# Performance work log

Hardware: AMD Instinct MI355X
Metric: run time of the kernel (lower is better)

## Reference

```python
import jax, jax.numpy as jnp
import numpy as np

INPUT_SIZE = 75
HIDDEN = 128
NUM_CLASSES = 10

def setup_inputs() -> dict:
    key = jax.random.key(0)
    ks = jax.random.split(key, 8)
    B, T = 512, 512
    s_ih = 1.0 / np.sqrt(HIDDEN)
    x = jax.random.normal(ks[0], (B, T, INPUT_SIZE), dtype=jnp.float32)
    w_ih = jax.random.uniform(ks[1], (4 * HIDDEN, INPUT_SIZE), jnp.float32, -s_ih, s_ih)
    w_hh = jax.random.uniform(ks[2], (4 * HIDDEN, HIDDEN), jnp.float32, -s_ih, s_ih)
    b_ih = jax.random.uniform(ks[3], (4 * HIDDEN,), jnp.float32, -s_ih, s_ih)
    b_hh = jax.random.uniform(ks[4], (4 * HIDDEN,), jnp.float32, -s_ih, s_ih)
    fc_w = jax.random.uniform(ks[5], (NUM_CLASSES, HIDDEN), jnp.float32, -s_ih, s_ih)
    fc_b = jax.random.uniform(ks[6], (NUM_CLASSES,), jnp.float32, -s_ih, s_ih)
    return {"x": x, "w_ih": w_ih, "w_hh": w_hh, "b_ih": b_ih, "b_hh": b_hh, "fc_w": fc_w, "fc_b": fc_b}

def _lstm_last_h(x, w_ih, w_hh, b_ih, b_hh):
    # x: [B, T, I]. Precompute input contribution once: [B, T, 4H]
    xg = jnp.einsum('bti,gi->btg', x, w_ih) + b_ih + b_hh
    B = x.shape[0]
    h0 = jnp.zeros((B, HIDDEN), x.dtype)
    c0 = jnp.zeros((B, HIDDEN), x.dtype)

    def step(carry, xg_t):
        h, c = carry
        gates = xg_t + h @ w_hh.T  # [B, 4H]
        i, f, g, o = jnp.split(gates, 4, axis=-1)  # torch gate order i,f,g,o
        i = jax.nn.sigmoid(i)
        f = jax.nn.sigmoid(f)
        g = jnp.tanh(g)
        o = jax.nn.sigmoid(o)
        c = f * c + i * g
        h = o * jnp.tanh(c)
        return (h, c), None

    (h, c), _ = jax.lax.scan(step, (h0, c0), jnp.swapaxes(xg, 0, 1))
    return h  # last hidden state [B, H]

def reference(x, w_ih, w_hh, b_ih, b_hh, fc_w, fc_b):
    h_n = _lstm_last_h(x, w_ih, w_hh, b_ih, b_hh)
    return h_n @ fc_w.T + fc_b  # [B, 10]
```

## Files before the change

### kernel.cpp

```cpp
#include <hip/hip_runtime.h>
#include <hip/hip_bf16.h>

#define HID 128
#define ISZ 75
#define KDIM 224
#define KC 7
#define TT 512
#define BB 512
#define ZSTR 232

typedef _Float16 half8 __attribute__((ext_vector_type(8)));
typedef float floatx4 __attribute__((ext_vector_type(4)));

__device__ __forceinline__ float rcp_fast(float x) { return __builtin_amdgcn_rcpf(x); }
__device__ __forceinline__ float sigmoid_f(float x) { return rcp_fast(1.f + __expf(-x)); }
__device__ __forceinline__ float tanh_f(float x) { return 1.f - 2.f * rcp_fast(__expf(2.f * x) + 1.f); }

__global__ __launch_bounds__(1024, 1) void lstm_mfma(
    const float* __restrict__ x,
    const float* __restrict__ w_ih,
    const float* __restrict__ w_hh,
    const float* __restrict__ b_ih,
    const float* __restrict__ b_hh,
    const float* __restrict__ fc_w,
    const float* __restrict__ fc_b,
    float* __restrict__ out)
{
    const int tid  = threadIdx.x;
    const int wave = tid >> 6;
    const int lane = tid & 63;
    const int l15  = lane & 15;
    const int l4   = lane >> 4;
    const int b0   = blockIdx.x * 2;
    const int wb   = wave * 32;

    __shared__ __align__(16) _Float16 zsh[16][ZSTR];
    __shared__ __align__(16) float    psh[2][512];

    {
        int* zi = (int*)&zsh[0][0];
        const int n4 = 16 * ZSTR / 2;
        for (int i = tid; i < n4; i += 1024) zi[i] = 0;
    }
    __syncthreads();

    if (tid >= 256 && tid < 256 + 2 * ISZ) {
        int u = tid - 256;
        int nb = (u >= ISZ) ? 1 : 0;
        int k = u - nb * ISZ;
        zsh[nb][HID + k] = (_Float16)x[((size_t)(b0 + nb) * TT) * ISZ + k];
    }

    half8  wfr[2][KC];
    floatx4 bias[2];
#pragma unroll
    for (int mt = 0; mt < 2; ++mt) {
        const int R = wb + mt * 16 + l15;
#pragma unroll
        for (int kc = 0; kc < KC; ++kc) {
            half8 f;
            const int kbase = kc * 32 + l4 * 8;
#pragma unroll
            for (int e = 0; e < 8; ++e) {
                const int k = kbase + e;
                float v = 0.f;
                if (k < HID)            v = w_hh[R * HID + k];
                else if (k < HID + ISZ) v = w_ih[R * ISZ + (k - HID)];
                f[e] = (_Float16)v;
            }
            wfr[mt][kc] = f;
        }
        floatx4 bf;
#pragma unroll
        for (int j = 0; j < 4; ++j) {
            const int g = wb + mt * 16 + l4 * 4 + j;
            bf[j] = b_ih[g] + b_hh[g];
        }
        bias[mt] = bf;
    }

    float c = 0.f;
    __syncthreads();

#pragma unroll 1
    for (int t = 0; t < TT; ++t) {
        float xpre = 0.f;
        int xnb = 0, xk = 0;
        const bool xthr = (tid >= 256 && tid < 256 + 2 * ISZ);
        if (xthr) {
            int u = tid - 256;
            xnb = (u >= ISZ) ? 1 : 0;
            xk = u - xnb * ISZ;
            int tn = (t + 1 < TT) ? (t + 1) : t;
            xpre = x[((size_t)(b0 + xnb) * TT + tn) * ISZ + xk];
        }

        floatx4 acc0 = bias[0], acc1 = bias[1];
#pragma unroll
        for (int kc = 0; kc < KC; ++kc) {
            half8 z = *(const half8*)&zsh[l15][kc * 32 + l4 * 8];
            acc0 = __builtin_amdgcn_mfma_f32_16x16x32_f16(wfr[0][kc], z, acc0, 0, 0, 0);
            acc1 = __builtin_amdgcn_mfma_f32_16x16x32_f16(wfr[1][kc], z, acc1, 0, 0, 0);
        }
        if (l15 < 2) {
            *(floatx4*)&psh[l15][wb + l4 * 4]      = acc0;
            *(floatx4*)&psh[l15][wb + 16 + l4 * 4] = acc1;
        }
        __syncthreads();

        if (tid < 256) {
            const int nb = tid >> 7, j = tid & 127;
            float pi = psh[nb][j];
            float pf = psh[nb][HID + j];
            float pg = psh[nb][2 * HID + j];
            float po = psh[nb][3 * HID + j];
            float ig = sigmoid_f(pi);
            float fg = sigmoid_f(pf);
            float gg = tanh_f(pg);
            float og = sigmoid_f(po);
            c = fmaf(fg, c, ig * gg);
            zsh[nb][j] = (_Float16)(og * tanh_f(c));
        } else if (xthr && (t + 1 < TT)) {
            zsh[xnb][HID + xk] = (_Float16)xpre;
        }
        __syncthreads();
    }

    if (tid < 20) {
        const int nb = tid / 10, k = tid - nb * 10;
        float s = fc_b[k];
        const float* w = fc_w + k * HID;
#pragma unroll
        for (int d = 0; d < HID; ++d) s = fmaf(w[d], (float)zsh[nb][d], s);
        out[(b0 + nb) * 10 + k] = s;
    }
}

extern "C" void kernel_launch(void* const* d_in, const int* in_sizes, int n_in,
                              void* d_out, int out_size, void* d_ws, size_t ws_size,
                              hipStream_t stream) {
    const float* x    = (const float*)d_in[0];
    const float* w_ih = (const float*)d_in[1];
    const float* w_hh = (const float*)d_in[2];
    const float* b_ih = (const float*)d_in[3];
    const float* b_hh = (const float*)d_in[4];
    const float* fc_w = (const float*)d_in[5];
    const float* fc_b = (const float*)d_in[6];
    float* out = (float*)d_out;

    lstm_mfma<<<dim3(BB / 2), dim3(1024), 0, stream>>>(
        x, w_ih, w_hh, b_ih, b_hh, fc_w, fc_b, out);
}
```

Before: 601.0 us.

## Precompute input projection with a separate GEMM kernel and shrink recurrent K

Adds an xg_gemm kernel that computes x·W_ih^T plus both biases for all timesteps into an fp16 workspace buffer. The recurrent kernel then only runs MFMAs over the 128-wide hidden state (4 K-chunks instead of 7) and prefetches the precomputed gate inputs two steps ahead. Hidden state in LDS moves to a chunk-interleaved layout. The cost is a 256 MB fp16 intermediate write and read through HBM, plus an extra kernel launch. The old fused kernel stays as a fallback when the workspace is too small.

```diff
diff --git a/kernel.cpp b/kernel.cpp
--- a/kernel.cpp
+++ b/kernel.cpp
@@ -3,36 +3,208 @@
 
 #define HID 128
 #define ISZ 75
-#define KDIM 224
-#define KC 7
+#define GATES 512
 #define TT 512
 #define BB 512
-#define ZSTR 232
 
 typedef _Float16 half8 __attribute__((ext_vector_type(8)));
+typedef _Float16 half4 __attribute__((ext_vector_type(4)));
 typedef float floatx4 __attribute__((ext_vector_type(4)));
 
 __device__ __forceinline__ float rcp_fast(float x) { return __builtin_amdgcn_rcpf(x); }
 __device__ __forceinline__ float sigmoid_f(float x) { return rcp_fast(1.f + __expf(-x)); }
 __device__ __forceinline__ float tanh_f(float x) { return 1.f - 2.f * rcp_fast(__expf(2.f * x) + 1.f); }
 
-__global__ __launch_bounds__(1024, 1) void lstm_mfma(
+__global__ __launch_bounds__(256, 2) void xg_gemm(
     const float* __restrict__ x,
     const float* __restrict__ w_ih,
-    const float* __restrict__ w_hh,
     const float* __restrict__ b_ih,
     const float* __restrict__ b_hh,
+    _Float16* __restrict__ xg)
+{
+    const int tid = threadIdx.x;
+    const int wv = tid >> 6, lane = tid & 63;
+    const int l15 = lane & 15, l4 = lane >> 4;
+
+    __shared__ __align__(16) _Float16 wlds[12 * 256 * 8];
+    __shared__ __align__(16) float    xlds[64 * ISZ];
+
+    const size_t rowblk = (size_t)blockIdx.x * 512;
+
+    for (int nh = 0; nh < 2; ++nh) {
+        const int gbase = nh * 256;
+        {
+            const float* wrow = w_ih + (size_t)(gbase + tid) * ISZ;
+            for (int k = 0; k < 96; ++k) {
+                float v = (k < ISZ) ? wrow[k] : 0.f;
+                wlds[((k >> 3) * 256 + tid) * 8 + (k & 7)] = (_Float16)v;
+            }
+        }
+        float biasv[16];
+#pragma unroll
+        for (int nt = 0; nt < 16; ++nt) {
+            int g = gbase + nt * 16 + l15;
+            biasv[nt] = b_ih[g] + b_hh[g];
+        }
+        __syncthreads();
+
+        for (int mt = 0; mt < 8; ++mt) {
+            const size_t r0 = rowblk + (size_t)mt * 64;
+            {
+                const float4* src = (const float4*)(x + r0 * ISZ);
+                float4* dst = (float4*)xlds;
+                for (int i = tid; i < 1200; i += 256) dst[i] = src[i];
+            }
+            __syncthreads();
+
+            half8 af[3];
+#pragma unroll
+            for (int kc = 0; kc < 3; ++kc) {
+                const int rb = (wv * 16 + l15) * ISZ;
+                half8 f;
+#pragma unroll
+                for (int e = 0; e < 8; ++e) {
+                    int k = kc * 32 + l4 * 8 + e;
+                    int kk = (k < ISZ) ? k : 0;
+                    float v = xlds[rb + kk];
+                    f[e] = (_Float16)((k < ISZ) ? v : 0.f);
+                }
+                af[kc] = f;
+            }
+
+            floatx4 acc[16];
+#pragma unroll
+            for (int nt = 0; nt < 16; ++nt)
+                acc[nt] = (floatx4){biasv[nt], biasv[nt], biasv[nt], biasv[nt]};
+#pragma unroll
+            for (int kc = 0; kc < 3; ++kc) {
+                const int cb = (kc * 4 + l4) * 256;
+#pragma unroll
+                for (int nt = 0; nt < 16; ++nt) {
+                    half8 bf = *(const half8*)&wlds[(cb + nt * 16 + l15) * 8];
+                    acc[nt] = __builtin_amdgcn_mfma_f32_16x16x32_f16(af[kc], bf, acc[nt], 0, 0, 0);
+                }
+            }
+
+            _Float16* orow = xg + (r0 + wv * 16 + l4 * 4) * GATES + gbase + l15;
+#pragma unroll
+            for (int nt = 0; nt < 16; ++nt) {
+#pragma unroll
+                for (int j = 0; j < 4; ++j)
+                    orow[(size_t)j * GATES + nt * 16] = (_Float16)acc[nt][j];
+            }
+            __syncthreads();
+        }
+        __syncthreads();
+    }
+}
+
+__global__ __launch_bounds__(1024, 1) void lstm_rec(
+    const _Float16* __restrict__ xg,
+    const float* __restrict__ w_hh,
     const float* __restrict__ fc_w,
     const float* __restrict__ fc_b,
     float* __restrict__ out)
 {
-    const int tid  = threadIdx.x;
-    const int wave = tid >> 6;
-    const int lane = tid & 63;
-    const int l15  = lane & 15;
-    const int l4   = lane >> 4;
-    const int b0   = blockIdx.x * 2;
-    const int wb   = wave * 32;
+    const int tid = threadIdx.x;
+    const int wave = tid >> 6, lane = tid & 63;
+    const int l15 = lane & 15, l4 = lane >> 4;
+    const int b0 = blockIdx.x * 2;
+    const int wb = wave * 32;
+
+    __shared__ __align__(16) _Float16 zsh[16 * 16 * 8];
+    __shared__ __align__(16) float    psh[2][GATES];
+
+    half8 wfr[2][4];
+#pragma unroll
+    for (int mt = 0; mt < 2; ++mt) {
+        const int R = wb + mt * 16 + l15;
+#pragma unroll
+        for (int kc = 0; kc < 4; ++kc) {
+            half8 f;
+#pragma unroll
+            for (int e = 0; e < 8; ++e)
+                f[e] = (_Float16)w_hh[R * HID + kc * 32 + l4 * 8 + e];
+            wfr[mt][kc] = f;
+        }
+    }
+    for (int i = tid; i < 16 * 16 * 8 / 2; i += 1024) ((uint32_t*)zsh)[i] = 0;
+
+    float c = 0.f;
+    const bool ldact = (l15 < 2);
+    const _Float16* xgp = xg + ((size_t)(b0 + (l15 & 1)) * TT) * GATES + wb + l4 * 4;
+
+    half4 xgA0, xgA1, xgB0, xgB1;
+    if (ldact) {
+        xgA0 = *(const half4*)(xgp);
+        xgA1 = *(const half4*)(xgp + 16);
+        xgB0 = *(const half4*)(xgp + GATES);
+        xgB1 = *(const half4*)(xgp + GATES + 16);
+    }
+    __syncthreads();
+
+    auto step = [&](half4& xq0, half4& xq1, int tpre) {
+        floatx4 acc0, acc1;
+#pragma unroll
+        for (int j = 0; j < 4; ++j) { acc0[j] = (float)xq0[j]; acc1[j] = (float)xq1[j]; }
+        if (ldact) {
+            const _Float16* p = xgp + (size_t)tpre * GATES;
+            xq0 = *(const half4*)(p);
+            xq1 = *(const half4*)(p + 16);
+        }
+#pragma unroll
+        for (int kc = 0; kc < 4; ++kc) {
+            half8 z = *(const half8*)&zsh[((kc * 4 + l4) * 16 + l15) * 8];
+            acc0 = __builtin_amdgcn_mfma_f32_16x16x32_f16(wfr[0][kc], z, acc0, 0, 0, 0);
+            acc1 = __builtin_amdgcn_mfma_f32_16x16x32_f16(wfr[1][kc], z, acc1, 0, 0, 0);
+        }
+        if (ldact) {
+            *(floatx4*)&psh[l15][wb + l4 * 4]      = acc0;
+            *(floatx4*)&psh[l15][wb + 16 + l4 * 4] = acc1;
+        }
+        __syncthreads();
+        if (tid < 256) {
+            const int nb = tid >> 7, j = tid & 127;
+            float ig = sigmoid_f(psh[nb][j]);
+            float fg = sigmoid_f(psh[nb][HID + j]);
+            float gg = tanh_f(psh[nb][2 * HID + j]);
+            float og = sigmoid_f(psh[nb][3 * HID + j]);
+            c = fmaf(fg, c, ig * gg);
+            zsh[((j >> 3) * 16 + nb) * 8 + (j & 7)] = (_Float16)(og * tanh_f(c));
+        }
+        __syncthreads();
+    };
+
+#pragma unroll 1
+    for (int t = 0; t < TT; t += 2) {
+        step(xgA0, xgA1, (t + 2 < TT) ? t + 2 : TT - 1);
+        step(xgB0, xgB1, (t + 3 < TT) ? t + 3 : TT - 1);
+    }
+
+    if (tid < 20) {
+        const int nb = tid / 10, k = tid - nb * 10;
+        float s = fc_b[k];
+        const float* w = fc_w + k * HID;
+#pragma unroll
+        for (int d = 0; d < HID; ++d)
+            s = fmaf(w[d], (float)zsh[((d >> 3) * 16 + nb) * 8 + (d & 7)], s);
+        out[(b0 + nb) * 10 + k] = s;
+    }
+}
+
+#define KC7 7
+#define ZSTR 232
+__global__ __launch_bounds__(1024, 1) void lstm_mfma(
+    const float* __restrict__ x, const float* __restrict__ w_ih,
+    const float* __restrict__ w_hh, const float* __restrict__ b_ih,
+    const float* __restrict__ b_hh, const float* __restrict__ fc_w,
+    const float* __restrict__ fc_b, float* __restrict__ out)
+{
+    const int tid = threadIdx.x;
+    const int wave = tid >> 6, lane = tid & 63;
+    const int l15 = lane & 15, l4 = lane >> 4;
+    const int b0 = blockIdx.x * 2;
+    const int wb = wave * 32;
 
     __shared__ __align__(16) _Float16 zsh[16][ZSTR];
     __shared__ __align__(16) float    psh[2][512];
@@ -43,21 +215,19 @@
         for (int i = tid; i < n4; i += 1024) zi[i] = 0;
     }
     __syncthreads();
-
     if (tid >= 256 && tid < 256 + 2 * ISZ) {
         int u = tid - 256;
         int nb = (u >= ISZ) ? 1 : 0;
         int k = u - nb * ISZ;
         zsh[nb][HID + k] = (_Float16)x[((size_t)(b0 + nb) * TT) * ISZ + k];
     }
-
-    half8  wfr[2][KC];
+    half8 wfr[2][KC7];
     floatx4 bias[2];
 #pragma unroll
     for (int mt = 0; mt < 2; ++mt) {
         const int R = wb + mt * 16 + l15;
 #pragma unroll
-        for (int kc = 0; kc < KC; ++kc) {
+        for (int kc = 0; kc < KC7; ++kc) {
             half8 f;
             const int kbase = kc * 32 + l4 * 8;
 #pragma unroll
@@ -78,10 +248,8 @@
         }
         bias[mt] = bf;
     }
-
     float c = 0.f;
     __syncthreads();
-
 #pragma unroll 1
     for (int t = 0; t < TT; ++t) {
         float xpre = 0.f;
@@ -94,10 +262,9 @@
             int tn = (t + 1 < TT) ? (t + 1) : t;
             xpre = x[((size_t)(b0 + xnb) * TT + tn) * ISZ + xk];
         }
-
         floatx4 acc0 = bias[0], acc1 = bias[1];
 #pragma unroll
-        for (int kc = 0; kc < KC; ++kc) {
+        for (int kc = 0; kc < KC7; ++kc) {
             half8 z = *(const half8*)&zsh[l15][kc * 32 + l4 * 8];
             acc0 = __builtin_amdgcn_mfma_f32_16x16x32_f16(wfr[0][kc], z, acc0, 0, 0, 0);
             acc1 = __builtin_amdgcn_mfma_f32_16x16x32_f16(wfr[1][kc], z, acc1, 0, 0, 0);
@@ -107,17 +274,12 @@
             *(floatx4*)&psh[l15][wb + 16 + l4 * 4] = acc1;
         }
         __syncthreads();
-
         if (tid < 256) {
             const int nb = tid >> 7, j = tid & 127;
-            float pi = psh[nb][j];
-            float pf = psh[nb][HID + j];
-            float pg = psh[nb][2 * HID + j];
-            float po = psh[nb][3 * HID + j];
-            float ig = sigmoid_f(pi);
-            float fg = sigmoid_f(pf);
-            float gg = tanh_f(pg);
-            float og = sigmoid_f(po);
+            float ig = sigmoid_f(psh[nb][j]);
+            float fg = sigmoid_f(psh[nb][HID + j]);
+            float gg = tanh_f(psh[nb][2 * HID + j]);
+            float og = sigmoid_f(psh[nb][3 * HID + j]);
             c = fmaf(fg, c, ig * gg);
             zsh[nb][j] = (_Float16)(og * tanh_f(c));
         } else if (xthr && (t + 1 < TT)) {
@@ -125,7 +287,6 @@
         }
         __syncthreads();
     }
-
     if (tid < 20) {
         const int nb = tid / 10, k = tid - nb * 10;
         float s = fc_b[k];
@@ -148,6 +309,13 @@
     const float* fc_b = (const float*)d_in[6];
     float* out = (float*)d_out;
 
-    lstm_mfma<<<dim3(BB / 2), dim3(1024), 0, stream>>>(
-        x, w_ih, w_hh, b_ih, b_hh, fc_w, fc_b, out);
+    const size_t xg_bytes = (size_t)BB * TT * GATES * sizeof(_Float16);
+    if (ws_size >= xg_bytes) {
+        _Float16* xg = (_Float16*)d_ws;
+        xg_gemm<<<dim3(512), dim3(256), 0, stream>>>(x, w_ih, b_ih, b_hh, xg);
+        lstm_rec<<<dim3(BB / 2), dim3(1024), 0, stream>>>(xg, w_hh, fc_w, fc_b, out);
+    } else {
+        lstm_mfma<<<dim3(BB / 2), dim3(1024), 0, stream>>>(
+            x, w_ih, w_hh, b_ih, b_hh, fc_w, fc_b, out);
+    }
 }
```

After: 658.0 us. +9.5%, slower.
